# Performance work log

Measured on AMD Instinct MI355X. Metric: run time of the kernel, lower is better.

The kernel has to match this reference:

```python
import jax, jax.numpy as jnp
import numpy as np

VOCAB = 16000   # code_size
EMBED = 16
HID = 256
B, T = 64, 128


def _glorot(key, shape, fan):
    return jax.random.normal(key, shape, dtype=jnp.float32) / np.sqrt(fan)


def setup_inputs() -> dict:
    key = jax.random.key(0)
    ks = jax.random.split(key, 20)
    inp = {
        "tokens": jax.random.randint(ks[0], (B, T), 0, VOCAB),
        "h0": jax.random.normal(ks[1], (B, HID), dtype=jnp.float32),
        "c0": jax.random.normal(ks[2], (B, HID), dtype=jnp.float32),
        "emb": jax.random.normal(ks[3], (VOCAB, EMBED), dtype=jnp.float32),
        # LSTMCell params, PyTorch layout: W_ih [4H, in], W_hh [4H, H], biases [4H]
        "Wih1": _glorot(ks[4], (4 * HID, EMBED), EMBED),
        "Whh1": _glorot(ks[5], (4 * HID, HID), HID),
        "bih1": jnp.zeros((4 * HID,), jnp.float32),
        "bhh1": jnp.zeros((4 * HID,), jnp.float32),
        "Wih2": _glorot(ks[6], (4 * HID, HID), HID),
        "Whh2": _glorot(ks[7], (4 * HID, HID), HID),
        "bih2": jnp.zeros((4 * HID,), jnp.float32),
        "bhh2": jnp.zeros((4 * HID,), jnp.float32),
        "Wih3": _glorot(ks[8], (4 * HID, HID), HID),
        "Whh3": _glorot(ks[9], (4 * HID, HID), HID),
        "bih3": jnp.zeros((4 * HID,), jnp.float32),
        "bhh3": jnp.zeros((4 * HID,), jnp.float32),
        # head: Linear(HID,HID) -> ReLU -> Linear(HID,VOCAB)
        "W1": _glorot(ks[10], (HID, HID), HID),
        "b1": jnp.zeros((HID,), jnp.float32),
        "W2": _glorot(ks[11], (VOCAB, HID), HID),
        "b2": jnp.zeros((VOCAB,), jnp.float32),
    }
    return inp


def _lstm_cell(x, h, c, Wih, Whh, bih, bhh):
    # PyTorch LSTMCell gate order: i, f, g, o
    gates = x @ Wih.T + bih + h @ Whh.T + bhh          # [B, 4H]
    i, f, g, o = jnp.split(gates, 4, axis=-1)
    i, f, o = jax.nn.sigmoid(i), jax.nn.sigmoid(f), jax.nn.sigmoid(o)
    g = jnp.tanh(g)
    c_new = f * c + i * g
    h_new = o * jnp.tanh(c_new)
    return h_new, c_new


def reference(tokens, h0, c0, emb,
              Wih1, Whh1, bih1, bhh1,
              Wih2, Whh2, bih2, bhh2,
              Wih3, Whh3, bih3, bhh3,
              W1, b1, W2, b2):
    Bn, Tn = tokens.shape
    x = emb[tokens]                       # [B, T, E]
    xs = jnp.swapaxes(x, 0, 1)            # [T, B, E] for scan over time

    def step(carry, x_t):
        h1, c1, h2, c2, h3, c3 = carry
        h1, c1 = _lstm_cell(x_t, h1, c1, Wih1, Whh1, bih1, bhh1)
        h2, c2 = _lstm_cell(h1, h2, c2, Wih2, Whh2, bih2, bhh2)
        h3, c3 = _lstm_cell(h2, h3, c3, Wih3, Whh3, bih3, bhh3)
        score = jax.nn.relu(h3 @ W1.T + b1) @ W2.T + b2   # [B, V]
        return (h1, c1, h2, c2, h3, c3), score

    init = (h0, c0, h0, c0, h0, c0)       # hidden1 = hidden2 = hidden3 = hidden
    _, scores = jax.lax.scan(step, init, xs)              # [T, B, V]
    scores = jnp.swapaxes(scores, 0, 1).reshape(Bn * Tn, -1)
    labels = tokens.reshape(-1)
    return scores, labels
```

## Files before the change

kernel.cpp:

```cpp
#include <hip/hip_runtime.h>
#include <hip/hip_bf16.h>
#include <stdint.h>

#define T_SEQ 128
#define BATCH 64
#define HIDN  256
#define EMB   16
#define VOCAB 16000
#define HSTR  40
#define POIS  0x7FC1

typedef __attribute__((ext_vector_type(8))) short short8v;
typedef __attribute__((ext_vector_type(4))) float f32x4;
typedef __attribute__((ext_vector_type(4))) int   i32x4;
typedef __attribute__((ext_vector_type(4))) unsigned short us4v;
typedef unsigned short ushort_t;

#define OFF_WC1    0
#define OFF_WC2    131072
#define OFF_WC3    393216
#define OFF_BS2    655360
#define OFF_BS3    656384
#define OFF_W1T    658432
#define OFF_H3     723968
#define OFF_S1     2821120
#define OFF_W2BF   3869696

#define OUT_XG     0
#define OUT_RINGS  8388608

#define RING_STRIDE 2113536
#define SLOT 16384

__device__ __forceinline__ ushort_t f2bf(float x) {
    __hip_bfloat16 h = __float2bfloat16(x);
    return *reinterpret_cast<ushort_t*>(&h);
}

__device__ __forceinline__ float dpp_x1(float x) {
    return __builtin_bit_cast(float, __builtin_amdgcn_mov_dpp(
        __builtin_bit_cast(int, x), 0xB1, 0xF, 0xF, true));
}
__device__ __forceinline__ float dpp_x2(float x) {
    return __builtin_bit_cast(float, __builtin_amdgcn_mov_dpp(
        __builtin_bit_cast(int, x), 0x4E, 0xF, 0xF, true));
}
__device__ __forceinline__ f32x4 dpp4_x1(f32x4 v) {
    f32x4 r; r[0]=dpp_x1(v[0]); r[1]=dpp_x1(v[1]); r[2]=dpp_x1(v[2]); r[3]=dpp_x1(v[3]); return r;
}
__device__ __forceinline__ f32x4 dpp4_x2(f32x4 v) {
    f32x4 r; r[0]=dpp_x2(v[0]); r[1]=dpp_x2(v[1]); r[2]=dpp_x2(v[2]); r[3]=dpp_x2(v[3]); return r;
}

__device__ __forceinline__ i32x4 bypass_ld128(const void* p) {
    i32x4 v;
    asm volatile("global_load_dwordx4 %0, %1, off sc0 sc1" : "=v"(v) : "v"((uint64_t)p));
    return v;
}
__device__ __forceinline__ void bypass_st128(void* p, f32x4 v) {
    asm volatile("global_store_dwordx4 %0, %1, off sc0 sc1" :: "v"((uint64_t)p), "v"(v) : "memory");
}
__device__ __forceinline__ void vm_drain() {
    asm volatile("s_waitcnt vmcnt(0)" ::: "memory");
    __builtin_amdgcn_sched_barrier(0);
}
__device__ __forceinline__ void lgkm_drain() {
    asm volatile("s_waitcnt lgkmcnt(0)" ::: "memory");
    __builtin_amdgcn_sched_barrier(0);
}

__global__ void k_poison(ushort_t* __restrict__ rbase) {
    unsigned int u = blockIdx.x * 256 + threadIdx.x;
    unsigned int l = u >> 20;
    unsigned int r = u & 1048575;
    unsigned int s = 1 + (r >> 13);
    unsigned int off = r & 8191;
    ((unsigned int*)(rbase + (size_t)l * RING_STRIDE + (size_t)s * SLOT))[off] = 0x7FC17FC1u;
}

__global__ void k_reorder_w(const float* __restrict__ Whh1,
                            const float* __restrict__ Wih2, const float* __restrict__ Whh2,
                            const float* __restrict__ Wih3, const float* __restrict__ Whh3,
                            float* __restrict__ wsf) {
    int bid = blockIdx.x;
    int layer = bid >> 10, c = bid & 1023;
    int wgi = c >> 7, rr = c & 127, jl = rr >> 2, gg = rr & 3;
    int row = gg * 256 + wgi * 32 + jl;
    int tid = threadIdx.x;
    if (layer == 0) {
        ushort_t* dst = (ushort_t*)(wsf + OFF_WC1) + (size_t)c * 256;
        dst[tid] = f2bf(Whh1[row * 256 + tid]);
    } else {
        const float* Wi = (layer == 1) ? Wih2 : Wih3;
        const float* Wh = (layer == 1) ? Whh2 : Whh3;
        ushort_t* dst = (ushort_t*)(wsf + ((layer == 1) ? OFF_WC2 : OFF_WC3)) + (size_t)c * 512;
        for (int k = tid; k < 512; k += 256)
            dst[k] = f2bf(k < 256 ? Wi[row * 256 + k] : Wh[row * 256 + k - 256]);
    }
}

__global__ void k_bias23(const float* __restrict__ bi2, const float* __restrict__ bh2,
                         const float* __restrict__ bi3, const float* __restrict__ bh3,
                         float* __restrict__ wsf) {
    int idx = blockIdx.x * 256 + threadIdx.x;
    int layer = idx >> 10, c = idx & 1023;
    int wgi = c >> 7, rr = c & 127, jl = rr >> 2, gg = rr & 3;
    int row = gg * 256 + wgi * 32 + jl;
    wsf[((layer == 0) ? OFF_BS2 : OFF_BS3) + c] =
        (layer == 0) ? (bi2[row] + bh2[row]) : (bi3[row] + bh3[row]);
}

__global__ void k_xg(const int* __restrict__ tokens, const float* __restrict__ emb,
                     const float* __restrict__ Wih1, const float* __restrict__ bih1,
                     const float* __restrict__ bhh1, float* __restrict__ xg) {
    int t = blockIdx.x, cg = blockIdx.y;
    int tid = threadIdx.x;
    __shared__ float xs[64][16];
    for (int idx = tid; idx < 1024; idx += 256) {
        int b = idx >> 4, e = idx & 15;
        xs[b][e] = emb[(size_t)tokens[b * T_SEQ + t] * 16 + e];
    }
    __syncthreads();
    int c = cg * 64 + (tid & 63);
    int b0 = (tid >> 6) * 16;
    int wgi = c >> 7, rr = c & 127, jl = rr >> 2, gg = rr & 3;
    int row = gg * 256 + wgi * 32 + jl;
    float wv[16];
    #pragma unroll
    for (int e = 0; e < 16; ++e) wv[e] = Wih1[row * 16 + e];
    float bias = bih1[row] + bhh1[row];
    float* dst = xg + ((size_t)t * 1024 + c) * 64 + b0;
    for (int b = 0; b < 16; ++b) {
        float s = bias;
        #pragma unroll
        for (int e = 0; e < 16; ++e) s += xs[b0 + b][e] * wv[e];
        dst[b] = s;
    }
}

__global__ void k_init_rings(const float* __restrict__ h0, ushort_t* __restrict__ rbase) {
    int idx = blockIdx.x * 256 + threadIdx.x;
    ushort_t v = f2bf(h0[idx]);
    rbase[idx] = v;
    rbase[RING_STRIDE + idx] = v;
    rbase[2 * RING_STRIDE + idx] = v;
}

__global__ void k_transpose_w1(const float* __restrict__ src, float* __restrict__ dst) {
    int idx = blockIdx.x * 256 + threadIdx.x;
    int n = idx & 255, k = idx >> 8;
    dst[idx] = src[n * 256 + k];
}

__global__ void k_conv_w2(const float* __restrict__ src, ushort_t* __restrict__ dst, int n) {
    int idx = blockIdx.x * 256 + threadIdx.x;
    if (idx < n) dst[idx] = f2bf(src[idx]);
}

template<int LAYER, int NKS>
__device__ __forceinline__ void lstm_body(
    int wg, int tid, const float* __restrict__ c0,
    float* __restrict__ wsf, float* __restrict__ outf,
    ushort_t* hA, ushort_t* hB, ushort_t* hS) {
    const int w = tid >> 6, lane = tid & 63, lr = lane & 15, lg = lane >> 4;
    const int g = lr & 3;
    const int K = NKS * 32;
    const ushort_t* WC = (const ushort_t*)(wsf + (LAYER == 0 ? OFF_WC1 : LAYER == 1 ? OFF_WC2 : OFF_WC3));
    ushort_t* H3b = (ushort_t*)(wsf + OFF_H3);
    const float* xg = outf + OUT_XG;
    ushort_t* rbase = (ushort_t*)(outf + OUT_RINGS);
    ushort_t* ringIn = rbase + (size_t)(LAYER == 0 ? 0 : LAYER - 1) * RING_STRIDE;
    ushort_t* ringOwn = rbase + (size_t)LAYER * RING_STRIDE;

    const int ccol = wg * 128 + 2 * w * 16 + lr;
    short8v wr0[NKS], wr1[NKS];
    #pragma unroll
    for (int ks = 0; ks < NKS; ++ks) {
        wr0[ks] = *(const short8v*)(WC + (size_t)ccol * K + ks * 32 + lg * 8);
        wr1[ks] = *(const short8v*)(WC + (size_t)(ccol + 16) * K + ks * 32 + lg * 8);
    }
    float bs0 = 0.f, bs1 = 0.f;
    if (LAYER > 0) {
        const float* BS = wsf + (LAYER == 1 ? OFF_BS2 : OFF_BS3);
        bs0 = BS[ccol]; bs1 = BS[ccol + 16];
    }
    const int jj0 = w * 8 + (lr >> 2);
    const int j0 = wg * 32 + jj0;
    f32x4 cst[4][2];
    #pragma unroll
    for (int i = 0; i < 4; ++i)
        #pragma unroll
        for (int r = 0; r < 4; ++r) {
            cst[i][0][r] = c0[(i * 16 + lg * 4 + r) * 256 + j0];
            cst[i][1][r] = c0[(i * 16 + lg * 4 + r) * 256 + j0 + 4];
        }

    const float sOwn = (g == 2) ? 2.f : -1.f;
    const float aOwn = (g == 2) ? -2.f : 1.f;
    const float bOwn = (g == 2) ? 1.f : 0.f;

    for (int t = 0; t < T_SEQ; ++t) {
        f32x4 xpre[8];
        if (LAYER == 0) {
            const float* xt = xg + ((size_t)t * 1024 + wg * 128) * 64;
            #pragma unroll
            for (int i = 0; i < 4; ++i) {
                xpre[i]     = *(const f32x4*)(xt + (size_t)(2 * w * 16 + lr) * 64 + i * 16 + lg * 4);
                xpre[i + 4] = *(const f32x4*)(xt + (size_t)((2 * w + 1) * 16 + lr) * 64 + i * 16 + lg * 4);
            }
        }
        i32x4 ta[8], tb[8];
        {
            const char* sA = (const char*)(LAYER == 0 ? (ringOwn + (size_t)t * SLOT)
                                                      : (ringIn + (size_t)(t + 1) * SLOT));
            const char* sB = (const char*)(ringOwn + (size_t)t * SLOT);
            bool bad;
            do {
                #pragma unroll
                for (int it = 0; it < 8; ++it)
                    ta[it] = bypass_ld128(sA + it * 4096 + tid * 16);
                if (LAYER > 0) {
                    #pragma unroll
                    for (int it = 0; it < 8; ++it)
                        tb[it] = bypass_ld128(sB + it * 4096 + tid * 16);
                }
                vm_drain();
                int p = 0;
                #pragma unroll
                for (int it = 0; it < 8; ++it)
                    p |= ((ta[it][0] & 0xFFFF) == POIS);
                if (LAYER > 0) {
                    #pragma unroll
                    for (int it = 0; it < 8; ++it)
                        p |= ((tb[it][0] & 0xFFFF) == POIS);
                }
                bad = __any(p);
            } while (bad);
        }
        __syncthreads();
        #pragma unroll
        for (int it = 0; it < 8; ++it) {
            int e16 = it * 256 + tid;
            int row = e16 >> 5, c16 = e16 & 31;
            int off = row * 512 + ((c16 ^ (row & 15)) << 4);
            *(i32x4*)((char*)hA + off) = ta[it];
            if (LAYER > 0) *(i32x4*)((char*)hB + off) = tb[it];
        }
        __syncthreads();
        f32x4 acc[4][2];
        if (LAYER == 0) {
            #pragma unroll
            for (int i = 0; i < 4; ++i) { acc[i][0] = xpre[i]; acc[i][1] = xpre[i + 4]; }
        } else {
            #pragma unroll
            for (int i = 0; i < 4; ++i) {
                acc[i][0] = (f32x4){bs0, bs0, bs0, bs0};
                acc[i][1] = (f32x4){bs1, bs1, bs1, bs1};
            }
        }
        #pragma unroll
        for (int i = 0; i < 4; ++i) {
            #pragma unroll
            for (int ks = 0; ks < NKS; ++ks) {
                const ushort_t* hsrc = (ks < 8) ? hA : hB;
                const int krem = ks & 7;
                short8v a = *(const short8v*)((const char*)hsrc + (i * 16 + lr) * 512 +
                                              (((krem * 4 + lg) ^ lr) << 4));
                acc[i][0] = __builtin_amdgcn_mfma_f32_16x16x32_bf16(a, wr0[ks], acc[i][0], 0, 0, 0);
                acc[i][1] = __builtin_amdgcn_mfma_f32_16x16x32_bf16(a, wr1[ks], acc[i][1], 0, 0, 0);
            }
        }
        #pragma unroll
        for (int i = 0; i < 4; ++i) {
            #pragma unroll
            for (int f = 0; f < 2; ++f) {
                f32x4 av = acc[i][f];
                f32x4 act;
                #pragma unroll
                for (int r = 0; r < 4; ++r) {
                    float e = __expf(sOwn * av[r]);
                    act[r] = fmaf(aOwn, __builtin_amdgcn_rcpf(1.f + e), bOwn);
                }
                f32x4 q1 = dpp4_x1(act), q2 = dpp4_x2(act), q3 = dpp4_x1(q2);
                f32x4 gI = (g == 0) ? act : (g == 1) ? q1 : (g == 2) ? q2 : q3;
                f32x4 gF = (g == 1) ? act : (g == 0) ? q1 : (g == 3) ? q2 : q3;
                f32x4 gG = (g == 2) ? act : (g == 3) ? q1 : (g == 0) ? q2 : q3;
                f32x4 gO = (g == 3) ? act : (g == 2) ? q1 : (g == 1) ? q2 : q3;
                f32x4 cv = gF * cst[i][f] + gI * gG;
                cst[i][f] = cv;
                float cg = (g == 0) ? cv[0] : (g == 1) ? cv[1] : (g == 2) ? cv[2] : cv[3];
                float go = (g == 0) ? gO[0] : (g == 1) ? gO[1] : (g == 2) ? gO[2] : gO[3];
                float e2 = __expf(2.f * cg);
                float th = fmaf(-2.f, __builtin_amdgcn_rcpf(1.f + e2), 1.f);
                float hval = go * th;
                int brow = i * 16 + lg * 4 + g;
                hS[brow * HSTR + jj0 + f * 4] = f2bf(hval);
            }
        }
        lgkm_drain();
        {
            f32x4 hv4 = *(const f32x4*)((const char*)hS + lane * (HSTR * 2) + w * 16);
            bypass_st128(ringOwn + (size_t)(t + 1) * SLOT + (size_t)lane * 256 + wg * 32 + w * 8, hv4);
            if (LAYER == 2)
                *(f32x4*)(H3b + (((size_t)lane * 128 + t) * 256 + wg * 32 + w * 8)) = hv4;
        }
    }
}

__global__ __launch_bounds__(256, 1) void k_lstm(const float* __restrict__ c0,
                                                 float* __restrict__ wsf,
                                                 float* __restrict__ outf) {
    __shared__ __align__(16) ushort_t hA[16384];
    __shared__ __align__(16) ushort_t hB[16384];
    __shared__ __align__(16) ushort_t hS[64 * HSTR];
    int layer = blockIdx.x >> 3, wg = blockIdx.x & 7;
    if (layer == 0)      lstm_body<0, 8>(wg, threadIdx.x, c0, wsf, outf, hA, hB, hS);
    else if (layer == 1) lstm_body<1, 16>(wg, threadIdx.x, c0, wsf, outf, hA, hB, hS);
    else                 lstm_body<2, 16>(wg, threadIdx.x, c0, wsf, outf, hA, hB, hS);
}

__global__ __launch_bounds__(256) void k_head1(const ushort_t* __restrict__ H3, const float* __restrict__ W1T,
                                               const float* __restrict__ b1, ushort_t* __restrict__ S1) {
    int tid = threadIdx.x;
    int r0 = blockIdx.x * 32;
    __shared__ float hs[32][256];
    {
        const short8v* src = (const short8v*)(H3 + (size_t)r0 * 256);
        float* hsf = &hs[0][0];
        for (int i = tid; i < 1024; i += 256) {
            short8v v = src[i];
            #pragma unroll
            for (int e = 0; e < 8; ++e) {
                unsigned int u = (unsigned int)(unsigned short)v[e];
                hsf[i * 8 + e] = __uint_as_float(u << 16);
            }
        }
    }
    __syncthreads();
    int c0i = (tid & 63) * 4;
    int rg = (tid >> 6) * 8;
    f32x4 bias = *(const f32x4*)(b1 + c0i);
    f32x4 acc[8];
    #pragma unroll
    for (int r = 0; r < 8; ++r) acc[r] = bias;
    for (int k = 0; k < 256; ++k) {
        f32x4 wv = *(const f32x4*)(W1T + (size_t)k * 256 + c0i);
        #pragma unroll
        for (int r = 0; r < 8; ++r) acc[r] += hs[rg + r][k] * wv;
    }
    #pragma unroll
    for (int r = 0; r < 8; ++r) {
        int row = r0 + rg + r;
        f32x4 v = acc[r];
        us4v u;
        u.x = f2bf(fmaxf(v[0], 0.f));
        u.y = f2bf(fmaxf(v[1], 0.f));
        u.z = f2bf(fmaxf(v[2], 0.f));
        u.w = f2bf(fmaxf(v[3], 0.f));
        *(us4v*)(S1 + (size_t)row * 256 + c0i) = u;
    }
}

__global__ __launch_bounds__(256) void k_head2(const ushort_t* __restrict__ S1,
                                               const ushort_t* __restrict__ W2,
                                               const float* __restrict__ b2, float* __restrict__ out) {
    __shared__ __align__(16) ushort_t As[128][32];
    __shared__ __align__(16) ushort_t Bs[128][32];
    int tid = threadIdx.x;
    int n0 = blockIdx.x * 128;
    int m0 = blockIdx.y * 128;
    int wave = tid >> 6, lane = tid & 63;
    int lr = lane & 15, lg = lane >> 4;
    int wm = (wave >> 1) * 64, wn = (wave & 1) * 64;
    f32x4 acc[4][4] = {};

    for (int kk = 0; kk < 256; kk += 32) {
        int id = tid;
        #pragma unroll
        for (int rep = 0; rep < 2; ++rep, id += 256) {
            int r = id >> 2, ch = (id & 3) * 8;
            *(short8v*)(&As[r][ch]) = *(const short8v*)(S1 + (size_t)(m0 + r) * 256 + kk + ch);
            *(short8v*)(&Bs[r][ch]) = *(const short8v*)(W2 + (size_t)(n0 + r) * 256 + kk + ch);
        }
        __syncthreads();
        short8v a[4], bb[4];
        #pragma unroll
        for (int i = 0; i < 4; ++i) a[i]  = *(const short8v*)(&As[wm + i * 16 + lr][lg * 8]);
        #pragma unroll
        for (int i = 0; i < 4; ++i) bb[i] = *(const short8v*)(&Bs[wn + i * 16 + lr][lg * 8]);
        #pragma unroll
        for (int i = 0; i < 4; ++i)
            #pragma unroll
            for (int f = 0; f < 4; ++f)
                acc[i][f] = __builtin_amdgcn_mfma_f32_16x16x32_bf16(a[i], bb[f], acc[i][f], 0, 0, 0);
        __syncthreads();
    }
    #pragma unroll
    for (int f = 0; f < 4; ++f) {
        int col = n0 + wn + f * 16 + lr;
        float bias = b2[col];
        #pragma unroll
        for (int i = 0; i < 4; ++i) {
            int rowb = m0 + wm + i * 16 + lg * 4;
            #pragma unroll
            for (int r = 0; r < 4; ++r)
                out[(size_t)(rowb + r) * VOCAB + col] = acc[i][f][r] + bias;
        }
    }
}

__global__ void k_labels(const int* __restrict__ tokens, float* __restrict__ out) {
    int i = blockIdx.x * 256 + threadIdx.x;
    if (i < BATCH * T_SEQ) out[i] = (float)tokens[i];
}

extern "C" void kernel_launch(void* const* d_in, const int* in_sizes, int n_in,
                              void* d_out, int out_size, void* d_ws, size_t ws_size,
                              hipStream_t stream) {
    const int*   tokens = (const int*)d_in[0];
    const float* h0   = (const float*)d_in[1];
    const float* c0   = (const float*)d_in[2];
    const float* emb  = (const float*)d_in[3];
    const float* Wih1 = (const float*)d_in[4];
    const float* Whh1 = (const float*)d_in[5];
    const float* bih1 = (const float*)d_in[6];
    const float* bhh1 = (const float*)d_in[7];
    const float* Wih2 = (const float*)d_in[8];
    const float* Whh2 = (const float*)d_in[9];
    const float* bih2 = (const float*)d_in[10];
    const float* bhh2 = (const float*)d_in[11];
    const float* Wih3 = (const float*)d_in[12];
    const float* Whh3 = (const float*)d_in[13];
    const float* bih3 = (const float*)d_in[14];
    const float* bhh3 = (const float*)d_in[15];
    const float* W1   = (const float*)d_in[16];
    const float* b1   = (const float*)d_in[17];
    const float* W2   = (const float*)d_in[18];
    const float* b2   = (const float*)d_in[19];

    float* ws  = (float*)d_ws;
    float* out = (float*)d_out;

    k_poison<<<12288, 256, 0, stream>>>((ushort_t*)(out + OUT_RINGS));
    k_reorder_w<<<3072, 256, 0, stream>>>(Whh1, Wih2, Whh2, Wih3, Whh3, ws);
    k_bias23<<<8, 256, 0, stream>>>(bih2, bhh2, bih3, bhh3, ws);
    k_xg<<<dim3(128, 16), 256, 0, stream>>>(tokens, emb, Wih1, bih1, bhh1, out + OUT_XG);
    k_init_rings<<<64, 256, 0, stream>>>(h0, (ushort_t*)(out + OUT_RINGS));
    k_transpose_w1<<<256, 256, 0, stream>>>(W1, ws + OFF_W1T);
    k_conv_w2<<<16000, 256, 0, stream>>>(W2, (ushort_t*)(ws + OFF_W2BF), VOCAB * 256);

    k_lstm<<<24, 256, 0, stream>>>(c0, ws, out);

    k_head1<<<256, 256, 0, stream>>>((const ushort_t*)(ws + OFF_H3), ws + OFF_W1T, b1, (ushort_t*)(ws + OFF_S1));
    dim3 g2(125, 64);
    k_head2<<<g2, 256, 0, stream>>>((const ushort_t*)(ws + OFF_S1),
                                    (const ushort_t*)(ws + OFF_W2BF), b2, out);
    k_labels<<<32, 256, 0, stream>>>(tokens, out + (size_t)BATCH * T_SEQ * VOCAB);
}
```

Measured before the change: 1.132 ms.

## Rewrite head1 as bf16 MFMA GEMM and vectorize W2 conversion

```diff
diff --git a/kernel.cpp b/kernel.cpp
--- a/kernel.cpp
+++ b/kernel.cpp
@@ -21,7 +21,7 @@
 #define OFF_WC3    393216
 #define OFF_BS2    655360
 #define OFF_BS3    656384
-#define OFF_W1T    658432
+#define OFF_W1BF   658432
 #define OFF_H3     723968
 #define OFF_S1     2821120
 #define OFF_W2BF   3869696
@@ -146,15 +146,23 @@
     rbase[2 * RING_STRIDE + idx] = v;
 }
 
-__global__ void k_transpose_w1(const float* __restrict__ src, float* __restrict__ dst) {
+__global__ void k_conv_w1(const float* __restrict__ W1, ushort_t* __restrict__ dst) {
     int idx = blockIdx.x * 256 + threadIdx.x;
-    int n = idx & 255, k = idx >> 8;
-    dst[idx] = src[n * 256 + k];
-}
-
-__global__ void k_conv_w2(const float* __restrict__ src, ushort_t* __restrict__ dst, int n) {
+    dst[idx] = f2bf(W1[idx]);
+}
+
+__global__ void k_conv_w2(const float* __restrict__ src, ushort_t* __restrict__ dst, int n8) {
     int idx = blockIdx.x * 256 + threadIdx.x;
-    if (idx < n) dst[idx] = f2bf(src[idx]);
+    if (idx < n8) {
+        f32x4 a = *(const f32x4*)(src + (size_t)idx * 8);
+        f32x4 b = *(const f32x4*)(src + (size_t)idx * 8 + 4);
+        short8v o;
+        o[0] = (short)f2bf(a[0]); o[1] = (short)f2bf(a[1]);
+        o[2] = (short)f2bf(a[2]); o[3] = (short)f2bf(a[3]);
+        o[4] = (short)f2bf(b[0]); o[5] = (short)f2bf(b[1]);
+        o[6] = (short)f2bf(b[2]); o[7] = (short)f2bf(b[3]);
+        *(short8v*)(dst + (size_t)idx * 8) = o;
+    }
 }
 
 template<int LAYER, int NKS>
@@ -319,45 +327,52 @@
     else                 lstm_body<2, 16>(wg, threadIdx.x, c0, wsf, outf, hA, hB, hS);
 }
 
-__global__ __launch_bounds__(256) void k_head1(const ushort_t* __restrict__ H3, const float* __restrict__ W1T,
-                                               const float* __restrict__ b1, ushort_t* __restrict__ S1) {
+__global__ __launch_bounds__(256) void k_head1m(const ushort_t* __restrict__ H3,
+                                                const ushort_t* __restrict__ W1B,
+                                                const float* __restrict__ b1,
+                                                ushort_t* __restrict__ S1) {
+    __shared__ __align__(16) ushort_t As[128][32];
+    __shared__ __align__(16) ushort_t Bs[128][32];
     int tid = threadIdx.x;
-    int r0 = blockIdx.x * 32;
-    __shared__ float hs[32][256];
-    {
-        const short8v* src = (const short8v*)(H3 + (size_t)r0 * 256);
-        float* hsf = &hs[0][0];
-        for (int i = tid; i < 1024; i += 256) {
-            short8v v = src[i];
-            #pragma unroll
-            for (int e = 0; e < 8; ++e) {
-                unsigned int u = (unsigned int)(unsigned short)v[e];
-                hsf[i * 8 + e] = __uint_as_float(u << 16);
-            }
-        }
-    }
-    __syncthreads();
-    int c0i = (tid & 63) * 4;
-    int rg = (tid >> 6) * 8;
-    f32x4 bias = *(const f32x4*)(b1 + c0i);
-    f32x4 acc[8];
+    int n0 = blockIdx.x * 128;
+    int m0 = blockIdx.y * 128;
+    int wave = tid >> 6, lane = tid & 63;
+    int lr = lane & 15, lg = lane >> 4;
+    int wm = (wave >> 1) * 64, wn = (wave & 1) * 64;
+    f32x4 acc[4][4] = {};
+
+    for (int kk = 0; kk < 256; kk += 32) {
+        int id = tid;
+        #pragma unroll
+        for (int rep = 0; rep < 2; ++rep, id += 256) {
+            int r = id >> 2, ch = (id & 3) * 8;
+            *(short8v*)(&As[r][ch]) = *(const short8v*)(H3 + (size_t)(m0 + r) * 256 + kk + ch);
+            *(short8v*)(&Bs[r][ch]) = *(const short8v*)(W1B + (size_t)(n0 + r) * 256 + kk + ch);
+        }
+        __syncthreads();
+        short8v a[4], bb[4];
+        #pragma unroll
+        for (int i = 0; i < 4; ++i) a[i]  = *(const short8v*)(&As[wm + i * 16 + lr][lg * 8]);
+        #pragma unroll
+        for (int i = 0; i < 4; ++i) bb[i] = *(const short8v*)(&Bs[wn + i * 16 + lr][lg * 8]);
+        #pragma unroll
+        for (int i = 0; i < 4; ++i)
+            #pragma unroll
+            for (int f = 0; f < 4; ++f)
+                acc[i][f] = __builtin_amdgcn_mfma_f32_16x16x32_bf16(a[i], bb[f], acc[i][f], 0, 0, 0);
+        __syncthreads();
+    }
     #pragma unroll
-    for (int r = 0; r < 8; ++r) acc[r] = bias;
-    for (int k = 0; k < 256; ++k) {
-        f32x4 wv = *(const f32x4*)(W1T + (size_t)k * 256 + c0i);
-        #pragma unroll
-        for (int r = 0; r < 8; ++r) acc[r] += hs[rg + r][k] * wv;
-    }
-    #pragma unroll
-    for (int r = 0; r < 8; ++r) {
-        int row = r0 + rg + r;
-        f32x4 v = acc[r];
-        us4v u;
-        u.x = f2bf(fmaxf(v[0], 0.f));
-        u.y = f2bf(fmaxf(v[1], 0.f));
-        u.z = f2bf(fmaxf(v[2], 0.f));
-        u.w = f2bf(fmaxf(v[3], 0.f));
-        *(us4v*)(S1 + (size_t)row * 256 + c0i) = u;
+    for (int f = 0; f < 4; ++f) {
+        int col = n0 + wn + f * 16 + lr;
+        float bias = b1[col];
+        #pragma unroll
+        for (int i = 0; i < 4; ++i) {
+            int rowb = m0 + wm + i * 16 + lg * 4;
+            #pragma unroll
+            for (int r = 0; r < 4; ++r)
+                S1[(size_t)(rowb + r) * 256 + col] = f2bf(fmaxf(acc[i][f][r] + bias, 0.f));
+        }
     }
 }
 
@@ -446,12 +461,15 @@
     k_bias23<<<8, 256, 0, stream>>>(bih2, bhh2, bih3, bhh3, ws);
     k_xg<<<dim3(128, 16), 256, 0, stream>>>(tokens, emb, Wih1, bih1, bhh1, out + OUT_XG);
     k_init_rings<<<64, 256, 0, stream>>>(h0, (ushort_t*)(out + OUT_RINGS));
-    k_transpose_w1<<<256, 256, 0, stream>>>(W1, ws + OFF_W1T);
-    k_conv_w2<<<16000, 256, 0, stream>>>(W2, (ushort_t*)(ws + OFF_W2BF), VOCAB * 256);
+    k_conv_w1<<<256, 256, 0, stream>>>(W1, (ushort_t*)(ws + OFF_W1BF));
+    k_conv_w2<<<2000, 256, 0, stream>>>(W2, (ushort_t*)(ws + OFF_W2BF), VOCAB * 256 / 8);
 
     k_lstm<<<24, 256, 0, stream>>>(c0, ws, out);
 
-    k_head1<<<256, 256, 0, stream>>>((const ushort_t*)(ws + OFF_H3), ws + OFF_W1T, b1, (ushort_t*)(ws + OFF_S1));
+    dim3 g1(2, 64);
+    k_head1m<<<g1, 256, 0, stream>>>((const ushort_t*)(ws + OFF_H3),
+                                     (const ushort_t*)(ws + OFF_W1BF), b1,
+                                     (ushort_t*)(ws + OFF_S1));
     dim3 g2(125, 64);
     k_head2<<<g2, 256, 0, stream>>>((const ushort_t*)(ws + OFF_S1),
                                     (const ushort_t*)(ws + OFF_W2BF), b2, out);
```

Result: no change. 1.115 ms (-1.5%).
